# Performance work log

Hardware: AMD Instinct MI355X
Metric: run time of the kernel (lower is better)

Reference implementation:

```python
import jax, jax.numpy as jnp
import numpy as np

B, S, R, A, DW, DR = 64, 32, 128, 64, 512, 512

def setup_inputs() -> dict:
    key = jax.random.key(0)
    ks = jax.random.split(key, 12)
    s = 0.02
    return {
        "b_question_vector": jax.random.normal(ks[0], (B, S, DW), jnp.float32),
        "b_question_mask": jnp.zeros((B, S), dtype=bool),  # True = padding
        "b_r_space": jax.random.randint(ks[1], (B, A), 0, R),
        "b_coverage_t": jax.random.uniform(ks[2], (B, S), jnp.float32),
        "rel_emb": jax.random.normal(ks[3], (R, DR), jnp.float32) * s,
        "Wq": jax.random.normal(ks[4], (DR, DW), jnp.float32) * s,
        "bq": jnp.zeros((DR,), jnp.float32),
        "Wr": jax.random.normal(ks[5], (DR, DR), jnp.float32) * s,
        "br": jnp.zeros((DR,), jnp.float32),
        "Wc": jax.random.normal(ks[6], (DR, 1), jnp.float32) * s,
        "bc": jnp.zeros((DR,), jnp.float32),
        "Watt": jax.random.normal(ks[7], (1, DR), jnp.float32) * s,
        "batt": jnp.zeros((1,), jnp.float32),
    }

def reference(b_question_vector, b_question_mask, b_r_space, b_coverage_t,
              rel_emb, Wq, bq, Wr, br, Wc, bc, Watt, batt):
    # question_linear: [B,S,DW] -> [B,S,DR] (computed once, not repeated R times)
    qp = jnp.einsum('bsw,dw->bsd', b_question_vector, Wq) + bq
    # relation_linear over full embedding table: [R,DR]
    rp = rel_emb @ Wr.T + br
    # coverage_linear: Linear(1, DR) applied to scalar coverage -> [B,S,DR]
    cp = b_coverage_t[:, :, None] * Wc[:, 0] + bc
    # additive attention features, broadcast instead of repeat+view: [B,R,S,DR]
    feat = jnp.tanh(qp[:, None, :, :] + rp[None, :, None, :] + cp[:, None, :, :])
    # W_att: [B,R,S,DR] -> [B,R,S]
    scores = jnp.einsum('brsd,d->brs', feat, Watt[0]) + batt[0]
    scores = jnp.where(b_question_mask[:, None, :], -jnp.inf, scores)
    alpha = jax.nn.softmax(scores, axis=-1)                      # softmax over seq
    ctx = jnp.einsum('brs,bsw->brw', alpha, b_question_vector)   # [B,R,DW]
    # per-batch gather output_i[relation_i] (vectorized)
    out = jnp.take_along_axis(ctx, b_r_space[:, :, None], axis=1)    # [B,A,DW]
    alpha_sel = jnp.take_along_axis(alpha, b_r_space[:, :, None], axis=1)  # [B,A,S]
    return (out, alpha_sel)
```

## Files before the change

kernel.cpp:

```cpp
#include <hip/hip_runtime.h>
#include <hip/hip_bf16.h>
#include <math.h>

#define B_  64
#define S_  32
#define R_  128
#define A_  64
#define DW_ 512
#define DR_ 512

__device__ __forceinline__ float fast_tanh(float x) {
    x = fminf(fmaxf(x, -15.0f), 15.0f);
    float e = __expf(2.0f * x);
    return fmaf(-2.0f, __builtin_amdgcn_rcpf(e + 1.0f), 1.0f);
}

__global__ __launch_bounds__(256) void gemm_dual_kernel(
    const float* __restrict__ A0, const float* __restrict__ B0, float* __restrict__ C0,
    int M0, int N0, int K0,
    const float* __restrict__ bias1_0, const float* __restrict__ bias2_0,
    const float* __restrict__ rowv0, const float* __restrict__ colv0,
    const float* __restrict__ A1, const float* __restrict__ B1, float* __restrict__ C1,
    int M1, int N1, int K1,
    const float* __restrict__ bias1_1)
{
    const int z = blockIdx.z;
    const float* Am; const float* Bm; float* C;
    const float *bias1, *bias2, *rowv, *colv;
    int M, N, K;
    if (z == 0) {
        Am = A0; Bm = B0; C = C0; M = M0; N = N0; K = K0;
        bias1 = bias1_0; bias2 = bias2_0; rowv = rowv0; colv = colv0;
    } else {
        Am = A1; Bm = B1; C = C1; M = M1; N = N1; K = K1;
        bias1 = bias1_1; bias2 = nullptr; rowv = nullptr; colv = nullptr;
    }

    const int bm = blockIdx.x * 64;
    const int bn = blockIdx.y * 64;
    if (bm >= M || bn >= N) return;

    __shared__ float As[16][64];
    __shared__ float Bs[16][64];
    const int tid = threadIdx.x;
    const int tr = tid >> 4;
    const int tc = tid & 15;
    const int lr = tid >> 2;
    const int lk = (tid & 3) << 2;
    float acc[4][4] = {};

    for (int k0 = 0; k0 < K; k0 += 16) {
        float4 av = *(const float4*)&Am[(size_t)(bm + lr) * K + k0 + lk];
        float4 bv = *(const float4*)&Bm[(size_t)(bn + lr) * K + k0 + lk];
        __syncthreads();
        As[lk + 0][lr] = av.x; As[lk + 1][lr] = av.y;
        As[lk + 2][lr] = av.z; As[lk + 3][lr] = av.w;
        Bs[lk + 0][lr] = bv.x; Bs[lk + 1][lr] = bv.y;
        Bs[lk + 2][lr] = bv.z; Bs[lk + 3][lr] = bv.w;
        __syncthreads();
        #pragma unroll
        for (int kk = 0; kk < 16; ++kk) {
            float4 a4 = *(const float4*)&As[kk][tr << 2];
            float4 b4 = *(const float4*)&Bs[kk][tc << 2];
            float aa[4] = {a4.x, a4.y, a4.z, a4.w};
            float bb[4] = {b4.x, b4.y, b4.z, b4.w};
            #pragma unroll
            for (int i = 0; i < 4; ++i)
                #pragma unroll
                for (int j = 0; j < 4; ++j)
                    acc[i][j] = fmaf(aa[i], bb[j], acc[i][j]);
        }
    }

    #pragma unroll
    for (int i = 0; i < 4; ++i) {
        const int m = bm + (tr << 2) + i;
        const float rv = rowv ? rowv[m] : 0.0f;
        float4 o;
        float* op = &o.x;
        #pragma unroll
        for (int j = 0; j < 4; ++j) {
            const int n = bn + (tc << 2) + j;
            float v = acc[i][j] + bias1[n];
            if (bias2) v += bias2[n];
            if (rowv)  v += rv * colv[n];
            op[j] = v;
        }
        *(float4*)&C[(size_t)m * N + bn + (tc << 2)] = o;
    }
}

__global__ __launch_bounds__(256) void attn_kernel(
    const float* __restrict__ u,
    const float* __restrict__ rp,
    const float* __restrict__ watt,
    const float* __restrict__ battp,
    const float* __restrict__ qv,
    const unsigned char* __restrict__ mask,
    const int* __restrict__ rspace,
    float* __restrict__ out,
    float* __restrict__ alpha_out)
{
    const int ba   = blockIdx.x;
    const int b    = ba >> 6;
    const int tid  = threadIdx.x;
    const int lane = tid & 63;
    const int wave = tid >> 6;
    const int r    = rspace[ba];

    __shared__ float s_scores[S_];
    __shared__ float s_alpha[S_];

    float rpv[8], wav[8];
    const float4* rp4 = (const float4*)(rp + (size_t)r * DR_);
    const float4* wa4 = (const float4*)watt;
    #pragma unroll
    for (int v = 0; v < 2; ++v) {
        float4 t = rp4[v * 64 + lane];
        float4 w = wa4[v * 64 + lane];
        rpv[v*4+0] = t.x; rpv[v*4+1] = t.y; rpv[v*4+2] = t.z; rpv[v*4+3] = t.w;
        wav[v*4+0] = w.x; wav[v*4+1] = w.y; wav[v*4+2] = w.z; wav[v*4+3] = w.w;
    }
    const float batt = battp[0];

    #pragma unroll
    for (int si = 0; si < 8; ++si) {
        const int s = (wave << 3) + si;
        const float4* u4 = (const float4*)(u + ((size_t)b * S_ + s) * DR_);
        float acc = 0.0f;
        #pragma unroll
        for (int v = 0; v < 2; ++v) {
            float4 uu = u4[v * 64 + lane];
            acc += wav[v*4+0] * fast_tanh(uu.x + rpv[v*4+0]);
            acc += wav[v*4+1] * fast_tanh(uu.y + rpv[v*4+1]);
            acc += wav[v*4+2] * fast_tanh(uu.z + rpv[v*4+2]);
            acc += wav[v*4+3] * fast_tanh(uu.w + rpv[v*4+3]);
        }
        #pragma unroll
        for (int off = 32; off > 0; off >>= 1)
            acc += __shfl_xor(acc, off);
        if (lane == 0) s_scores[s] = acc + batt;
    }
    __syncthreads();

    if (tid < S_) {
        float sc = s_scores[tid];
        if (mask[b * S_ + tid]) sc = -INFINITY;
        float m = sc;
        #pragma unroll
        for (int off = 16; off > 0; off >>= 1)
            m = fmaxf(m, __shfl_xor(m, off));
        float e = __expf(sc - m);
        float sum = e;
        #pragma unroll
        for (int off = 16; off > 0; off >>= 1)
            sum += __shfl_xor(sum, off);
        float al = e / sum;
        s_alpha[tid] = al;
        alpha_out[(size_t)ba * S_ + tid] = al;
    }
    __syncthreads();

    float2 acc2 = make_float2(0.0f, 0.0f);
    const float* qb = qv + (size_t)b * S_ * DW_;
    #pragma unroll 4
    for (int s = 0; s < S_; ++s) {
        const float al = s_alpha[s];
        float2 q = *(const float2*)&qb[s * DW_ + tid * 2];
        acc2.x = fmaf(al, q.x, acc2.x);
        acc2.y = fmaf(al, q.y, acc2.y);
    }
    *(float2*)&out[(size_t)ba * DW_ + tid * 2] = acc2;
}

extern "C" void kernel_launch(void* const* d_in, const int* in_sizes, int n_in,
                              void* d_out, int out_size, void* d_ws, size_t ws_size,
                              hipStream_t stream) {
    const float*         qv   = (const float*)d_in[0];
    const unsigned char* mask = (const unsigned char*)d_in[1];
    const int*           rsp  = (const int*)d_in[2];
    const float*         cov  = (const float*)d_in[3];
    const float*         rel  = (const float*)d_in[4];
    const float*         Wq   = (const float*)d_in[5];
    const float*         bq   = (const float*)d_in[6];
    const float*         Wr   = (const float*)d_in[7];
    const float*         br   = (const float*)d_in[8];
    const float*         Wc   = (const float*)d_in[9];
    const float*         bc   = (const float*)d_in[10];
    const float*         Watt = (const float*)d_in[11];
    const float*         batt = (const float*)d_in[12];

    float* u  = (float*)d_ws;
    float* rp = u + (size_t)B_ * S_ * DR_;

    float* out       = (float*)d_out;
    float* alpha_out = out + (size_t)B_ * A_ * DW_;

    dim3 blk(256);

    gemm_dual_kernel<<<dim3((B_ * S_) / 64, DR_ / 64, 2), blk, 0, stream>>>(
        qv, Wq, u, B_ * S_, DR_, DW_, bq, bc, cov, Wc,
        rel, Wr, rp, R_, DR_, DR_, br);

    attn_kernel<<<dim3(B_ * A_), blk, 0, stream>>>(
        u, rp, Watt, batt, qv, mask, rsp, out, alpha_out);
}
```

Before: 147.7 us.

## Use split-bf16 MFMA with swizzled LDS in projection GEMM

Result: faster. 127.5 us (-13.7%).

```diff
diff --git a/kernel.cpp b/kernel.cpp
--- a/kernel.cpp
+++ b/kernel.cpp
@@ -9,10 +9,27 @@
 #define DW_ 512
 #define DR_ 512
 
+typedef __attribute__((ext_vector_type(8))) short short8;
+typedef __attribute__((ext_vector_type(4))) float f32x4;
+
 __device__ __forceinline__ float fast_tanh(float x) {
     x = fminf(fmaxf(x, -15.0f), 15.0f);
     float e = __expf(2.0f * x);
     return fmaf(-2.0f, __builtin_amdgcn_rcpf(e + 1.0f), 1.0f);
+}
+
+__device__ __forceinline__ unsigned short bf16_rn(float x) {
+    union { float f; unsigned u; } v; v.f = x;
+    unsigned r = v.u + 0x7FFF + ((v.u >> 16) & 1);
+    return (unsigned short)(r >> 16);
+}
+__device__ __forceinline__ float bf16_to_f(unsigned short h) {
+    union { unsigned u; float f; } v; v.u = ((unsigned)h) << 16;
+    return v.f;
+}
+
+__device__ __forceinline__ int swz(int row, int chunk) {
+    return row * 32 + ((chunk ^ ((row >> 1) & 3)) << 3);
 }
 
 __global__ __launch_bounds__(256) void gemm_dual_kernel(
@@ -40,54 +57,96 @@
     const int bn = blockIdx.y * 64;
     if (bm >= M || bn >= N) return;
 
-    __shared__ float As[16][64];
-    __shared__ float Bs[16][64];
-    const int tid = threadIdx.x;
-    const int tr = tid >> 4;
-    const int tc = tid & 15;
-    const int lr = tid >> 2;
-    const int lk = (tid & 3) << 2;
-    float acc[4][4] = {};
-
-    for (int k0 = 0; k0 < K; k0 += 16) {
-        float4 av = *(const float4*)&Am[(size_t)(bm + lr) * K + k0 + lk];
-        float4 bv = *(const float4*)&Bm[(size_t)(bn + lr) * K + k0 + lk];
+    __shared__ unsigned short Ahi[64 * 32], Alo[64 * 32];
+    __shared__ unsigned short Bhi[64 * 32], Blo[64 * 32];
+
+    const int tid  = threadIdx.x;
+    const int l    = tid & 63;
+    const int w    = tid >> 6;
+    const int wr   = w >> 1;
+    const int wc   = w & 1;
+    const int fr   = l & 15;
+    const int fc   = l >> 4;
+    const int srow = tid >> 2;
+    const int sch  = tid & 3;
+
+    f32x4 acc[2][2] = {};
+
+    float4 ra0, ra1, rb0, rb1;
+    {
+        const size_t arow = (size_t)(bm + srow) * K + sch * 8;
+        const size_t brow = (size_t)(bn + srow) * K + sch * 8;
+        ra0 = *(const float4*)&Am[arow];     ra1 = *(const float4*)&Am[arow + 4];
+        rb0 = *(const float4*)&Bm[brow];     rb1 = *(const float4*)&Bm[brow + 4];
+    }
+
+    const int nsteps = K >> 5;
+    for (int s = 0; s < nsteps; ++s) {
+        short8 ahi, alo, bhi, blo;
+        {
+            float af[8] = {ra0.x, ra0.y, ra0.z, ra0.w, ra1.x, ra1.y, ra1.z, ra1.w};
+            float bf[8] = {rb0.x, rb0.y, rb0.z, rb0.w, rb1.x, rb1.y, rb1.z, rb1.w};
+            #pragma unroll
+            for (int e = 0; e < 8; ++e) {
+                unsigned short h = bf16_rn(af[e]);
+                ahi[e] = (short)h;
+                alo[e] = (short)bf16_rn(af[e] - bf16_to_f(h));
+                unsigned short g = bf16_rn(bf[e]);
+                bhi[e] = (short)g;
+                blo[e] = (short)bf16_rn(bf[e] - bf16_to_f(g));
+            }
+        }
         __syncthreads();
-        As[lk + 0][lr] = av.x; As[lk + 1][lr] = av.y;
-        As[lk + 2][lr] = av.z; As[lk + 3][lr] = av.w;
-        Bs[lk + 0][lr] = bv.x; Bs[lk + 1][lr] = bv.y;
-        Bs[lk + 2][lr] = bv.z; Bs[lk + 3][lr] = bv.w;
+        *(short8*)&Ahi[swz(srow, sch)] = ahi;
+        *(short8*)&Alo[swz(srow, sch)] = alo;
+        *(short8*)&Bhi[swz(srow, sch)] = bhi;
+        *(short8*)&Blo[swz(srow, sch)] = blo;
         __syncthreads();
-        #pragma unroll
-        for (int kk = 0; kk < 16; ++kk) {
-            float4 a4 = *(const float4*)&As[kk][tr << 2];
-            float4 b4 = *(const float4*)&Bs[kk][tc << 2];
-            float aa[4] = {a4.x, a4.y, a4.z, a4.w};
-            float bb[4] = {b4.x, b4.y, b4.z, b4.w};
+
+        if (s + 1 < nsteps) {
+            const int k0 = (s + 1) << 5;
+            const size_t arow = (size_t)(bm + srow) * K + k0 + sch * 8;
+            const size_t brow = (size_t)(bn + srow) * K + k0 + sch * 8;
+            ra0 = *(const float4*)&Am[arow];     ra1 = *(const float4*)&Am[arow + 4];
+            rb0 = *(const float4*)&Bm[brow];     rb1 = *(const float4*)&Bm[brow + 4];
+        }
+
+        short8 fahi[2], falo[2], fbhi[2], fblo[2];
+        #pragma unroll
+        for (int i = 0; i < 2; ++i) {
+            const int r = wr * 32 + i * 16 + fr;
+            fahi[i] = *(const short8*)&Ahi[swz(r, fc)];
+            falo[i] = *(const short8*)&Alo[swz(r, fc)];
+            const int c = wc * 32 + i * 16 + fr;
+            fbhi[i] = *(const short8*)&Bhi[swz(c, fc)];
+            fblo[i] = *(const short8*)&Blo[swz(c, fc)];
+        }
+        #pragma unroll
+        for (int i = 0; i < 2; ++i)
             #pragma unroll
-            for (int i = 0; i < 4; ++i)
-                #pragma unroll
-                for (int j = 0; j < 4; ++j)
-                    acc[i][j] = fmaf(aa[i], bb[j], acc[i][j]);
-        }
+            for (int j = 0; j < 2; ++j) {
+                acc[i][j] = __builtin_amdgcn_mfma_f32_16x16x32_bf16(fahi[i], fbhi[j], acc[i][j], 0, 0, 0);
+                acc[i][j] = __builtin_amdgcn_mfma_f32_16x16x32_bf16(fahi[i], fblo[j], acc[i][j], 0, 0, 0);
+                acc[i][j] = __builtin_amdgcn_mfma_f32_16x16x32_bf16(falo[i], fbhi[j], acc[i][j], 0, 0, 0);
+            }
     }
 
     #pragma unroll
-    for (int i = 0; i < 4; ++i) {
-        const int m = bm + (tr << 2) + i;
-        const float rv = rowv ? rowv[m] : 0.0f;
-        float4 o;
-        float* op = &o.x;
-        #pragma unroll
-        for (int j = 0; j < 4; ++j) {
-            const int n = bn + (tc << 2) + j;
-            float v = acc[i][j] + bias1[n];
-            if (bias2) v += bias2[n];
-            if (rowv)  v += rv * colv[n];
-            op[j] = v;
-        }
-        *(float4*)&C[(size_t)m * N + bn + (tc << 2)] = o;
-    }
+    for (int i = 0; i < 2; ++i)
+        #pragma unroll
+        for (int j = 0; j < 2; ++j) {
+            const int n  = bn + wc * 32 + j * 16 + fr;
+            const float b1 = bias1[n];
+            const float b2 = bias2 ? bias2[n] : 0.0f;
+            const float cv = colv ? colv[n] : 0.0f;
+            #pragma unroll
+            for (int reg = 0; reg < 4; ++reg) {
+                const int m = bm + wr * 32 + i * 16 + fc * 4 + reg;
+                float v = acc[i][j][reg] + b1 + b2;
+                if (rowv) v += rowv[m] * cv;
+                C[(size_t)m * N + n] = v;
+            }
+        }
 }
 
 __global__ __launch_bounds__(256) void attn_kernel(
```
